# Kernel optimization log

Measured on AMD Instinct MI355X. Metric: run time of the kernel, lower is better.

Reference implementation:

```python
import jax, jax.numpy as jnp
import numpy as np

N = 50000
E = 800000
T = 16
F_NODE = 8
VOCAB = 30000
D_TXT = 64
H = 64
C = 2


def _gru_last(emb, w_ih, w_hh, b_ih, b_hh):
    # emb: [N, T, D_TXT] -> last hidden state [N, H] (PyTorch GRU equations)
    def step(h, xt):
        gi = xt @ w_ih.T + b_ih          # [N, 3H]
        gh = h @ w_hh.T + b_hh           # [N, 3H]
        i_r, i_z, i_n = jnp.split(gi, 3, axis=-1)
        h_r, h_z, h_n = jnp.split(gh, 3, axis=-1)
        r = jax.nn.sigmoid(i_r + h_r)
        z = jax.nn.sigmoid(i_z + h_z)
        n = jnp.tanh(i_n + r * h_n)
        h_new = (1.0 - z) * n + z * h
        return h_new, None
    h0 = jnp.zeros((emb.shape[0], H), dtype=emb.dtype)
    hT, _ = jax.lax.scan(step, h0, jnp.swapaxes(emb, 0, 1))
    return hT


def _gcn_norm(edge_index, n_nodes):
    # add self-loops, symmetric normalization (PyG GCNConv default)
    loops = jnp.arange(n_nodes, dtype=edge_index.dtype)
    row = jnp.concatenate([edge_index[0], loops])
    col = jnp.concatenate([edge_index[1], loops])
    deg = jax.ops.segment_sum(jnp.ones_like(col, dtype=jnp.float32), col,
                              num_segments=n_nodes)
    dinv = jax.lax.rsqrt(jnp.maximum(deg, 1.0))
    norm = dinv[row] * dinv[col]
    return row, col, norm


def _gcn_conv(x, row, col, norm, W, b, n_nodes):
    m = x @ W                                    # [N, H]
    msg = norm[:, None] * m[row]                 # gather + scale
    out = jax.ops.segment_sum(msg, col, num_segments=n_nodes)
    return out + b


def setup_inputs() -> dict:
    key = jax.random.key(0)
    ks = jax.random.split(key, 16)
    s = 0.05
    return {
        "x": jax.random.normal(ks[0], (N, F_NODE), dtype=jnp.float32),
        "edge_index": jax.random.randint(ks[1], (2, E), 0, N, dtype=jnp.int32),
        "xtext": jax.random.randint(ks[2], (N, T), 0, VOCAB, dtype=jnp.int32),
        "embed": jax.random.normal(ks[3], (VOCAB, D_TXT), dtype=jnp.float32),
        "w_ih": jax.random.normal(ks[4], (3 * H, D_TXT), dtype=jnp.float32) * s,
        "w_hh": jax.random.normal(ks[5], (3 * H, H), dtype=jnp.float32) * s,
        "b_ih": jnp.zeros((3 * H,), dtype=jnp.float32),
        "b_hh": jnp.zeros((3 * H,), dtype=jnp.float32),
        "W1": jax.random.normal(ks[6], (F_NODE + H, H), dtype=jnp.float32) * s,
        "b1": jnp.zeros((H,), dtype=jnp.float32),
        "W2": jax.random.normal(ks[7], (H, H), dtype=jnp.float32) * s,
        "b2": jnp.zeros((H,), dtype=jnp.float32),
        "Wl1": jax.random.normal(ks[8], (2 * H, H), dtype=jnp.float32) * s,
        "bl1": jnp.zeros((H,), dtype=jnp.float32),
        "Wf": jax.random.normal(ks[9], (H, C), dtype=jnp.float32) * s,
        "bf": jnp.zeros((C,), dtype=jnp.float32),
    }


def reference(x, edge_index, xtext, embed, w_ih, w_hh, b_ih, b_hh,
              W1, b1, W2, b2, Wl1, bl1, Wf, bf):
    n_nodes = x.shape[0]
    # text encode: embedding lookup + GRU, take last timestep
    emb = embed[xtext]                               # [N, T, D_TXT]
    textout = _gru_last(emb, w_ih, w_hh, b_ih, b_hh)  # [N, H]
    h = jnp.concatenate([x, textout], axis=1)        # [N, F_NODE+H]
    # two GCN layers with shared normalized edge structure
    row, col, norm = _gcn_norm(edge_index, n_nodes)
    h = jax.nn.relu(_gcn_conv(h, row, col, norm, W1, b1, n_nodes))
    h = jax.nn.relu(_gcn_conv(h, row, col, norm, W2, b2, n_nodes))
    # edge-pair classifier (original edges, no self-loops)
    xpair = jnp.concatenate([h[edge_index[0]], h[edge_index[1]]], axis=1)
    xpair = jax.nn.relu(xpair @ Wl1 + bl1)
    logits = xpair @ Wf + bf
    return jax.nn.log_softmax(logits, axis=1)
```

## Files before the change

kernel.cpp:

```cpp
#include <hip/hip_runtime.h>
#include <math.h>

#define N_NODES 50000
#define N_EDGES 800000
#define SCAN_NB ((N_NODES + 255) / 256)
#define VOCAB   30000
#define NT32    ((N_NODES + 31) / 32)

typedef __attribute__((ext_vector_type(8)))  short bf16x8;
typedef __attribute__((ext_vector_type(4)))  float f32x4;
typedef __attribute__((ext_vector_type(16))) float f32x16;
typedef __attribute__((ext_vector_type(4)))  int   i32x4;

__device__ inline short f2bf(float f) {
    union { float f; unsigned u; } v; v.f = f;
    unsigned r = v.u + 0x7FFFu + ((v.u >> 16) & 1u);
    return (short)(r >> 16);
}
__device__ inline float bflo(unsigned u) { union { unsigned u; float f; } v; v.u = u << 16; return v.f; }
__device__ inline float bfhi(unsigned u) { union { unsigned u; float f; } v; v.u = u & 0xffff0000u; return v.f; }
__device__ inline unsigned cvtpk(float a, float b) {
    unsigned r; asm("v_cvt_pk_bf16_f32 %0, %1, %2" : "=v"(r) : "v"(a), "v"(b)); return r;
}
__device__ inline float exp2neg(float x) { float r; asm("v_exp_f32 %0, -%1" : "=v"(r) : "v"(x)); return r; }
__device__ inline float exp2p(float x)   { float r; asm("v_exp_f32 %0, %1"  : "=v"(r) : "v"(x)); return r; }

__device__ inline f32x4 mfma16(bf16x8 a, bf16x8 b, f32x4 c) {
    return __builtin_amdgcn_mfma_f32_16x16x32_bf16(a, b, c, 0, 0, 0);
}
__device__ inline f32x16 mfma32(bf16x8 a, bf16x8 b, f32x16 c) {
    return __builtin_amdgcn_mfma_f32_32x32x16_bf16(a, b, c, 0, 0, 0);
}
__device__ inline f32x16 splat16(float v) {
    f32x16 r;
    #pragma unroll
    for (int i = 0; i < 16; ++i) r[i] = v;
    return r;
}
__device__ inline bf16x8 asbf(i32x4 v) { union { i32x4 i; bf16x8 b; } u; u.i = v; return u.b; }

__global__ void k_embcvt(const float* __restrict__ e, short* __restrict__ o) {
    int i = blockIdx.x * 256 + threadIdx.x;
    if (i >= VOCAB * 64 / 8) return;
    const float4* p = (const float4*)(e + i * 8);
    float4 a = p[0], b = p[1];
    bf16x8 v;
    v[0]=f2bf(a.x); v[1]=f2bf(a.y); v[2]=f2bf(a.z); v[3]=f2bf(a.w);
    v[4]=f2bf(b.x); v[5]=f2bf(b.y); v[6]=f2bf(b.z); v[7]=f2bf(b.w);
    *(bf16x8*)(o + i * 8) = v;
}

__global__ void k_count(const int* __restrict__ ei, int* __restrict__ cnt) {
    int e = blockIdx.x * 256 + threadIdx.x;
    if (e < N_EDGES) atomicAdd(&cnt[ei[N_EDGES + e]], 1);
}
__global__ void k_scan_local(const int* __restrict__ cnt, int* __restrict__ excl,
                             int* __restrict__ bsum) {
    __shared__ int s[256];
    int tid = threadIdx.x;
    int i = blockIdx.x * 256 + tid;
    int v = (i < N_NODES) ? cnt[i] : 0;
    s[tid] = v;
    __syncthreads();
    #pragma unroll
    for (int off = 1; off < 256; off <<= 1) {
        int t = (tid >= off) ? s[tid - off] : 0;
        __syncthreads();
        s[tid] += t;
        __syncthreads();
    }
    if (i < N_NODES) excl[i] = s[tid] - v;
    if (tid == 255) bsum[blockIdx.x] = s[255];
}
__global__ void k_scan_bsum(int* __restrict__ bsum) {
    __shared__ int s[256];
    int tid = threadIdx.x;
    int v = (tid < SCAN_NB) ? bsum[tid] : 0;
    s[tid] = v;
    __syncthreads();
    #pragma unroll
    for (int off = 1; off < 256; off <<= 1) {
        int t = (tid >= off) ? s[tid - off] : 0;
        __syncthreads();
        s[tid] += t;
        __syncthreads();
    }
    if (tid < SCAN_NB) bsum[tid] = s[tid] - v;
}
__global__ void k_make_starts(const int* __restrict__ excl, const int* __restrict__ bsum,
                              const int* __restrict__ cnt,
                              int* __restrict__ starts, int* __restrict__ cursor,
                              float* __restrict__ dinv) {
    int i = blockIdx.x * 256 + threadIdx.x;
    if (i >= N_NODES) return;
    int st = excl[i] + bsum[blockIdx.x];
    starts[i] = st;
    cursor[i] = st;
    dinv[i] = rsqrtf((float)cnt[i] + 1.0f);
}
__global__ void k_fill(const int* __restrict__ ei, int* __restrict__ cursor,
                       int* __restrict__ csr_src) {
    int e = blockIdx.x * 256 + threadIdx.x;
    if (e >= N_EDGES) return;
    int c = ei[N_EDGES + e];
    int p = atomicAdd(&cursor[c], 1);
    csr_src[p] = ei[e];
}

__global__ __launch_bounds__(256) void k_gru8(
    const int*   __restrict__ xtext,
    const short* __restrict__ embbf,
    const float* __restrict__ w_ih, const float* __restrict__ w_hh,
    const float* __restrict__ b_ih, const float* __restrict__ b_hh,
    unsigned* __restrict__ ht32)
{
    __shared__ short bfrag[2 * 4 * 6 * 64 * 8];
    __shared__ short hbuf[4][32 * 64];

    const int tid = threadIdx.x;
    const float L2E = 1.4426950408889634f;
    for (int u = tid; u < 3072; u += 256) {
        int l   = u & 63;
        int ct  = (u >> 6) % 6;
        int ks  = (u / 384) % 4;
        int mat = u / 1536;
        const float* W = mat ? w_hh : w_ih;
        float sc = (ct < 4) ? L2E : 2.0f * L2E;
        const float* src = &W[(ct * 32 + (l & 31)) * 64 + ks * 16 + ((l >> 5) << 3)];
        short* dst = &bfrag[u * 8];
        #pragma unroll
        for (int i = 0; i < 8; ++i) dst[i] = f2bf(src[i] * sc);
    }
    __syncthreads();

    const int lane = tid & 63;
    const int wave = tid >> 6;
    const int l5 = lane >> 5;
    const int cl = lane & 31;

    const int tile  = blockIdx.x * 4 + wave;
    if (tile >= NT32) return;
    const int nbase = tile * 32;

    float b_r[2], b_z[2], b_ni[2], b_nh[2];
    #pragma unroll
    for (int p = 0; p < 2; ++p) {
        int j = p * 32 + cl;
        b_r[p]  = (b_ih[j]        + b_hh[j])        * L2E;
        b_z[p]  = (b_ih[64 + j]   + b_hh[64 + j])   * L2E;
        b_ni[p] = b_ih[128 + j] * (2.0f * L2E);
        b_nh[p] = b_hh[128 + j] * (2.0f * L2E);
    }

    const bf16x8* BF = (const bf16x8*)bfrag;
    short* hl = &hbuf[wave][0];

    float hr0[16], hr1[16];
    #pragma unroll
    for (int g = 0; g < 16; ++g) { hr0[g] = 0.0f; hr1[g] = 0.0f; }

    const int node = min(nbase + cl, N_NODES - 1);
    const int* toks = &xtext[node * 16];

    bf16x8 eA[4], eB[4];

#define LOADE(DST, T) { int tok_ = toks[T]; const short* er_ = &embbf[tok_ * 64 + 8 * l5]; \
    DST[0] = *(const bf16x8*)(er_);      DST[1] = *(const bf16x8*)(er_ + 16); \
    DST[2] = *(const bf16x8*)(er_ + 32); DST[3] = *(const bf16x8*)(er_ + 48); }

#define STEP(T, EC, EP, FIRST, LAST) { \
    bf16x8 hA[4]; \
    if (!(FIRST)) { \
        _Pragma("unroll") \
        for (int ks = 0; ks < 4; ++ks) { \
            int o = (ks * 2 + l5) ^ (cl & 7); \
            hA[ks] = *(const bf16x8*)&hl[cl * 64 + o * 8]; \
        } \
    } \
    if (!(LAST)) LOADE(EP, (T) + 1); \
    _Pragma("unroll") \
    for (int p = 0; p < 2; ++p) { \
        f32x16 ar = splat16(b_r[p]); \
        f32x16 az = splat16(b_z[p]); \
        f32x16 ai = splat16(b_ni[p]); \
        f32x16 ah = splat16(b_nh[p]); \
        _Pragma("unroll") \
        for (int ks = 0; ks < 4; ++ks) { \
            ar = mfma32(EC[ks], BF[(ks * 6 + p) * 64 + lane], ar); \
            az = mfma32(EC[ks], BF[(ks * 6 + 2 + p) * 64 + lane], az); \
            ai = mfma32(EC[ks], BF[(ks * 6 + 4 + p) * 64 + lane], ai); \
        } \
        if (!(FIRST)) { \
            _Pragma("unroll") \
            for (int ks = 0; ks < 4; ++ks) { \
                ar = mfma32(hA[ks], BF[((4 + ks) * 6 + p) * 64 + lane], ar); \
                az = mfma32(hA[ks], BF[((4 + ks) * 6 + 2 + p) * 64 + lane], az); \
                ah = mfma32(hA[ks], BF[((4 + ks) * 6 + 4 + p) * 64 + lane], ah); \
            } \
        } \
        float* hrp = p ? hr1 : hr0; \
        _Pragma("unroll") \
        for (int g = 0; g < 16; ++g) { \
            float r = __builtin_amdgcn_rcpf(1.0f + exp2neg(ar[g])); \
            float z = __builtin_amdgcn_rcpf(1.0f + exp2neg(az[g])); \
            float v = ai[g] + r * ah[g]; \
            float n = 1.0f - 2.0f * __builtin_amdgcn_rcpf(exp2p(v) + 1.0f); \
            hrp[g] = n + z * (hrp[g] - n); \
        } \
    } \
    _Pragma("unroll") \
    for (int g = 0; g < 16; ++g) { \
        unsigned u = cvtpk(hr0[g], hr1[g]); \
        int m = (g & 3) + 8 * (g >> 2) + 4 * l5; \
        if (!(LAST)) { \
            int o0 = (cl >> 3) ^ (m & 7); \
            int o1 = (4 + (cl >> 3)) ^ (m & 7); \
            hl[m * 64 + o0 * 8 + (cl & 7)] = (short)u; \
            hl[m * 64 + o1 * 8 + (cl & 7)] = (short)(u >> 16); \
        } else { \
            int n_ = nbase + m; \
            if (n_ < N_NODES) ht32[(unsigned)n_ * 32 + cl] = u; \
        } \
    } \
}

    LOADE(eA, 0);
    STEP(0, eA, eB, true, false)

    #pragma unroll 1
    for (int tt = 0; tt < 7; ++tt) {
        int t1 = 1 + 2 * tt;
        STEP(t1,     eB, eA, false, false)
        STEP(t1 + 1, eA, eB, false, false)
    }
    STEP(15, eB, eA, false, true)

#undef STEP
#undef LOADE
}

__global__ __launch_bounds__(256) void k_mm1_mf(
    const float* __restrict__ x, const unsigned* __restrict__ ht32,
    const float* __restrict__ W1, const float* __restrict__ dinv,
    unsigned* __restrict__ msb)
{
    __shared__ short bfw[2 * 5 * 64 * 8];
    const int tid = threadIdx.x;
    for (int u = tid; u < 640; u += 256) {
        int l = u & 63, f = u >> 6;
        int ks = f % 5, p = f / 5;
        int c = p * 32 + (l & 31);
        int wl5 = l >> 5;
        short* dst = &bfw[u * 8];
        if (ks < 4) {
            const float* src = &W1[(8 + ks * 16 + 8 * wl5) * 64 + c];
            #pragma unroll
            for (int i = 0; i < 8; ++i) dst[i] = f2bf(src[i * 64]);
        } else {
            #pragma unroll
            for (int i = 0; i < 8; ++i) dst[i] = (wl5 == 0) ? f2bf(W1[i * 64 + c]) : (short)0;
        }
    }
    __syncthreads();

    const int lane = tid & 63;
    const int wave = tid >> 6;
    const int l5 = lane >> 5;
    const int cl = lane & 31;
    const int tile = blockIdx.x * 4 + wave;
    if (tile >= NT32) return;
    const int nbase = tile * 32;
    const int node = min(nbase + cl, N_NODES - 1);

    const uint4* hp = (const uint4*)(ht32 + (unsigned)node * 32);
    uint4 A0 = hp[2 * l5], A1 = hp[2 * l5 + 1];
    uint4 A2 = hp[4 + 2 * l5], A3 = hp[5 + 2 * l5];
    const float4* xp = (const float4*)(x + (size_t)node * 8);
    float4 x0 = xp[0], x1 = xp[1];

    unsigned w0[8] = {A0.x, A0.y, A0.z, A0.w, A1.x, A1.y, A1.z, A1.w};
    unsigned w1[8] = {A2.x, A2.y, A2.z, A2.w, A3.x, A3.y, A3.z, A3.w};

    bf16x8 fa[5];
    {
        i32x4 t;
        #pragma unroll
        for (int i = 0; i < 4; ++i) t[i] = (int)((w0[2*i] & 0xffffu) | (w0[2*i+1] << 16));
        fa[0] = asbf(t);
        #pragma unroll
        for (int i = 0; i < 4; ++i) t[i] = (int)((w1[2*i] & 0xffffu) | (w1[2*i+1] << 16));
        fa[1] = asbf(t);
        #pragma unroll
        for (int i = 0; i < 4; ++i) t[i] = (int)((w0[2*i] >> 16) | (w0[2*i+1] & 0xffff0000u));
        fa[2] = asbf(t);
        #pragma unroll
        for (int i = 0; i < 4; ++i) t[i] = (int)((w1[2*i] >> 16) | (w1[2*i+1] & 0xffff0000u));
        fa[3] = asbf(t);
        if (l5 == 0) {
            t[0] = (int)cvtpk(x0.x, x0.y); t[1] = (int)cvtpk(x0.z, x0.w);
            t[2] = (int)cvtpk(x1.x, x1.y); t[3] = (int)cvtpk(x1.z, x1.w);
        } else {
            t[0] = t[1] = t[2] = t[3] = 0;
        }
        fa[4] = asbf(t);
    }

    const bf16x8* BW = (const bf16x8*)bfw;
    f32x16 a0 = (f32x16)(0.0f), a1 = (f32x16)(0.0f);
    #pragma unroll
    for (int ks = 0; ks < 5; ++ks) {
        a0 = mfma32(fa[ks], BW[ks * 64 + lane], a0);
        a1 = mfma32(fa[ks], BW[(5 + ks) * 64 + lane], a1);
    }

    #pragma unroll
    for (int g = 0; g < 16; ++g) {
        int m = (g & 3) + 8 * (g >> 2) + 4 * l5;
        int n = nbase + m;
        if (n < N_NODES) {
            float dv = dinv[n];
            msb[(unsigned)n * 32 + cl] = cvtpk(a0[g] * dv, a1[g] * dv);
        }
    }
}

__global__ __launch_bounds__(256) void k_mm2_mf(
    const unsigned* __restrict__ h1b, const float* __restrict__ W2,
    const float* __restrict__ dinv, unsigned* __restrict__ msb)
{
    __shared__ short bfw[2 * 4 * 64 * 8];
    const int tid = threadIdx.x;
    for (int u = tid; u < 512; u += 256) {
        int l = u & 63, f = u >> 6;
        int ks = f & 3, p = f >> 2;
        int c = p * 32 + (l & 31);
        int wl5 = l >> 5;
        const float* src = &W2[(ks * 16 + 8 * wl5) * 64 + c];
        short* dst = &bfw[u * 8];
        #pragma unroll
        for (int i = 0; i < 8; ++i) dst[i] = f2bf(src[i * 64]);
    }
    __syncthreads();

    const int lane = tid & 63;
    const int wave = tid >> 6;
    const int l5 = lane >> 5;
    const int cl = lane & 31;
    const int tile = blockIdx.x * 4 + wave;
    if (tile >= NT32) return;
    const int nbase = tile * 32;
    const int node = min(nbase + cl, N_NODES - 1);

    const uint4* hp = (const uint4*)(h1b + (unsigned)node * 32);
    uint4 A0 = hp[2 * l5], A1 = hp[2 * l5 + 1];
    uint4 A2 = hp[4 + 2 * l5], A3 = hp[5 + 2 * l5];

    unsigned w0[8] = {A0.x, A0.y, A0.z, A0.w, A1.x, A1.y, A1.z, A1.w};
    unsigned w1[8] = {A2.x, A2.y, A2.z, A2.w, A3.x, A3.y, A3.z, A3.w};

    bf16x8 fa[4];
    {
        i32x4 t;
        #pragma unroll
        for (int i = 0; i < 4; ++i) t[i] = (int)((w0[2*i] & 0xffffu) | (w0[2*i+1] << 16));
        fa[0] = asbf(t);
        #pragma unroll
        for (int i = 0; i < 4; ++i) t[i] = (int)((w1[2*i] & 0xffffu) | (w1[2*i+1] << 16));
        fa[1] = asbf(t);
        #pragma unroll
        for (int i = 0; i < 4; ++i) t[i] = (int)((w0[2*i] >> 16) | (w0[2*i+1] & 0xffff0000u));
        fa[2] = asbf(t);
        #pragma unroll
        for (int i = 0; i < 4; ++i) t[i] = (int)((w1[2*i] >> 16) | (w1[2*i+1] & 0xffff0000u));
        fa[3] = asbf(t);
    }

    const bf16x8* BW = (const bf16x8*)bfw;
    f32x16 a0 = (f32x16)(0.0f), a1 = (f32x16)(0.0f);
    #pragma unroll
    for (int ks = 0; ks < 4; ++ks) {
        a0 = mfma32(fa[ks], BW[ks * 64 + lane], a0);
        a1 = mfma32(fa[ks], BW[(4 + ks) * 64 + lane], a1);
    }

    #pragma unroll
    for (int g = 0; g < 16; ++g) {
        int m = (g & 3) + 8 * (g >> 2) + 4 * l5;
        int n = nbase + m;
        if (n < N_NODES) {
            float dv = dinv[n];
            msb[(unsigned)n * 32 + cl] = cvtpk(a0[g] * dv, a1[g] * dv);
        }
    }
}

__global__ __launch_bounds__(256) void k_gather_p(
    const unsigned* __restrict__ msb, const int* __restrict__ csr_src,
    const int* __restrict__ starts, const int* __restrict__ cnt,
    const float* __restrict__ dinv, const float* __restrict__ b,
    unsigned* __restrict__ outp)
{
    int n = blockIdx.x * 8 + (threadIdx.x >> 5);
    if (n >= N_NODES) return;
    int w = threadIdx.x & 31;
    int c = cnt[n];
    const int* lst = csr_src + starts[n];
    unsigned us = msb[(unsigned)n * 32 + w];
    float a0 = bflo(us), a1 = bfhi(us);
    int k = 0;
    for (; k + 4 <= c; k += 4) {
        int r0 = lst[k], r1 = lst[k+1], r2 = lst[k+2], r3 = lst[k+3];
        unsigned u0 = msb[(unsigned)r0 * 32 + w];
        unsigned u1 = msb[(unsigned)r1 * 32 + w];
        unsigned u2 = msb[(unsigned)r2 * 32 + w];
        unsigned u3 = msb[(unsigned)r3 * 32 + w];
        a0 += bflo(u0) + bflo(u1) + bflo(u2) + bflo(u3);
        a1 += bfhi(u0) + bfhi(u1) + bfhi(u2) + bfhi(u3);
    }
    for (; k < c; ++k) {
        unsigned u = msb[(unsigned)lst[k] * 32 + w];
        a0 += bflo(u); a1 += bfhi(u);
    }
    float d = dinv[n];
    float v0 = fmaxf(d * a0 + b[w], 0.0f);
    float v1 = fmaxf(d * a1 + b[w + 32], 0.0f);
    outp[(unsigned)n * 32 + w] = cvtpk(v0, v1);
}

__global__ __launch_bounds__(256) void k_gather_h2(
    const unsigned* __restrict__ msb, const int* __restrict__ csr_src,
    const int* __restrict__ starts, const int* __restrict__ cnt,
    const float* __restrict__ dinv, const float* __restrict__ b,
    short* __restrict__ out)
{
    int n = blockIdx.x * 8 + (threadIdx.x >> 5);
    if (n >= N_NODES) return;
    int w = threadIdx.x & 31;
    int c = cnt[n];
    const int* lst = csr_src + starts[n];
    unsigned us = msb[(unsigned)n * 32 + w];
    float a0 = bflo(us), a1 = bfhi(us);
    int k = 0;
    for (; k + 4 <= c; k += 4) {
        int r0 = lst[k], r1 = lst[k+1], r2 = lst[k+2], r3 = lst[k+3];
        unsigned u0 = msb[(unsigned)r0 * 32 + w];
        unsigned u1 = msb[(unsigned)r1 * 32 + w];
        unsigned u2 = msb[(unsigned)r2 * 32 + w];
        unsigned u3 = msb[(unsigned)r3 * 32 + w];
        a0 += bflo(u0) + bflo(u1) + bflo(u2) + bflo(u3);
        a1 += bfhi(u0) + bfhi(u1) + bfhi(u2) + bfhi(u3);
    }
    for (; k < c; ++k) {
        unsigned u = msb[(unsigned)lst[k] * 32 + w];
        a0 += bflo(u); a1 += bfhi(u);
    }
    float d = dinv[n];
    float v0 = fmaxf(d * a0 + b[w], 0.0f);
    float v1 = fmaxf(d * a1 + b[w + 32], 0.0f);
    unsigned u = cvtpk(v0, v1);
    out[(unsigned)n * 64 + w]      = (short)u;
    out[(unsigned)n * 64 + 32 + w] = (short)(u >> 16);
}

__global__ __launch_bounds__(256) void k_edge_mfma(
    const int* __restrict__ ei, const short* __restrict__ h2b,
    const float* __restrict__ Wl1, const float* __restrict__ bl1,
    const float* __restrict__ Wf,  const float* __restrict__ bf,
    float* __restrict__ out)
{
    __shared__ float wl_s[128 * 64];
    const int tid = threadIdx.x;
    for (int i = tid; i < 128 * 64; i += 256) wl_s[i] = Wl1[i];
    __syncthreads();

    const int lane = tid & 63;
    const int wave = tid >> 6;
    const int lg = lane >> 4;
    const int ll = lane & 15;

    bf16x8 B[16];
    #pragma unroll
    for (int ks = 0; ks < 4; ++ks) {
        #pragma unroll
        for (int ct = 0; ct < 4; ++ct) {
            int c  = ct * 16 + ll;
            int kb = ks * 32 + 8 * lg;
            bf16x8 v;
            #pragma unroll
            for (int i = 0; i < 8; ++i) v[i] = f2bf(wl_s[(kb + i) * 64 + c]);
            B[ks * 4 + ct] = v;
        }
    }
    float wf0[4], wf1[4], bl[4];
    #pragma unroll
    for (int ct = 0; ct < 4; ++ct) {
        int c = ct * 16 + ll;
        wf0[ct] = Wf[c * 2 + 0];
        wf1[ct] = Wf[c * 2 + 1];
        bl[ct]  = bl1[c];
    }
    const float bf0 = bf[0], bf1 = bf[1];

    for (int tile = blockIdx.x * 4 + wave; tile < N_EDGES / 16; tile += gridDim.x * 4) {
        const int ebase = tile * 16;
        const int erow  = ebase + ll;
        const int src = ei[erow];
        const int dst = ei[N_EDGES + erow];

        f32x4 acc[4];
        #pragma unroll
        for (int ct = 0; ct < 4; ++ct) acc[ct] = (f32x4){bl[ct], bl[ct], bl[ct], bl[ct]};

        #pragma unroll
        for (int ks = 0; ks < 4; ++ks) {
            const int nd = (ks < 2) ? src : dst;
            bf16x8 A = *(const bf16x8*)&h2b[nd * 64 + (ks & 1) * 32 + 8 * lg];
            #pragma unroll
            for (int ct = 0; ct < 4; ++ct) acc[ct] = mfma16(A, B[ks * 4 + ct], acc[ct]);
        }

        float p0[4], p1[4];
        #pragma unroll
        for (int q = 0; q < 4; ++q) { p0[q] = 0.0f; p1[q] = 0.0f; }
        #pragma unroll
        for (int ct = 0; ct < 4; ++ct) {
            #pragma unroll
            for (int q = 0; q < 4; ++q) {
                float hd = fmaxf(acc[ct][q], 0.0f);
                p0[q] += hd * wf0[ct];
                p1[q] += hd * wf1[ct];
            }
        }
        #pragma unroll
        for (int m = 1; m <= 8; m <<= 1) {
            #pragma unroll
            for (int q = 0; q < 4; ++q) {
                p0[q] += __shfl_xor(p0[q], m, 64);
                p1[q] += __shfl_xor(p1[q], m, 64);
            }
        }
        if (ll < 8) {
            int q = ll >> 1, cls = ll & 1;
            float l0 = p0[q] + bf0, l1 = p1[q] + bf1;
            float mx  = fmaxf(l0, l1);
            float lse = mx + __logf(__expf(l0 - mx) + __expf(l1 - mx));
            float val = (cls ? l1 : l0) - lse;
            out[(ebase + 4 * lg + q) * 2 + cls] = val;
        }
    }
}

extern "C" void kernel_launch(void* const* d_in, const int* in_sizes, int n_in,
                              void* d_out, int out_size, void* d_ws, size_t ws_size,
                              hipStream_t stream) {
    const float* x     = (const float*)d_in[0];
    const int*   ei    = (const int*)  d_in[1];
    const int*   xtext = (const int*)  d_in[2];
    const float* embed = (const float*)d_in[3];
    const float* w_ih  = (const float*)d_in[4];
    const float* w_hh  = (const float*)d_in[5];
    const float* b_ih  = (const float*)d_in[6];
    const float* b_hh  = (const float*)d_in[7];
    const float* W1    = (const float*)d_in[8];
    const float* b1    = (const float*)d_in[9];
    const float* W2    = (const float*)d_in[10];
    const float* b2    = (const float*)d_in[11];
    const float* Wl1   = (const float*)d_in[12];
    const float* bl1   = (const float*)d_in[13];
    const float* Wf    = (const float*)d_in[14];
    const float* bf    = (const float*)d_in[15];
    float* out = (float*)d_out;

    char* ws = (char*)d_ws;
    size_t off = 0;
    auto alloc = [&](size_t bytes) { char* p = ws + off; off += (bytes + 255) & ~size_t(255); return p; };
    unsigned* ht32   = (unsigned*)alloc(N_NODES * 32 * 4);
    unsigned* msb    = (unsigned*)alloc(N_NODES * 32 * 4);
    unsigned* h1b    = (unsigned*)alloc(N_NODES * 32 * 4);
    short*    h2b    = (short*)   alloc(N_NODES * 64 * 2);
    float*    dinv   = (float*)   alloc(N_NODES * 4);
    int*      cnt    = (int*)     alloc(N_NODES * 4);
    int*      excl   = (int*)     alloc(N_NODES * 4);
    int*      starts = (int*)     alloc(N_NODES * 4);
    int*      cursor = (int*)     alloc(N_NODES * 4);
    int*      bsum   = (int*)     alloc(SCAN_NB * 4);
    int*      csr_src= (int*)     alloc(N_EDGES * 4);
    short*    embbf  = (short*)   alloc(VOCAB * 64 * 2);

    k_embcvt<<<(VOCAB * 64 / 8 + 255) / 256, 256, 0, stream>>>(embed, embbf);

    hipMemsetAsync(cnt, 0, N_NODES * 4, stream);
    k_count<<<(N_EDGES + 255) / 256, 256, 0, stream>>>(ei, cnt);
    k_scan_local<<<SCAN_NB, 256, 0, stream>>>(cnt, excl, bsum);
    k_scan_bsum<<<1, 256, 0, stream>>>(bsum);
    k_make_starts<<<SCAN_NB, 256, 0, stream>>>(excl, bsum, cnt, starts, cursor, dinv);
    k_fill<<<(N_EDGES + 255) / 256, 256, 0, stream>>>(ei, cursor, csr_src);

    k_gru8<<<(NT32 + 3) / 4, 256, 0, stream>>>(xtext, embbf, w_ih, w_hh, b_ih, b_hh, ht32);

    k_mm1_mf<<<(NT32 + 3) / 4, 256, 0, stream>>>(x, ht32, W1, dinv, msb);
    k_gather_p<<<(N_NODES + 7) / 8, 256, 0, stream>>>(msb, csr_src, starts, cnt, dinv, b1, h1b);

    k_mm2_mf<<<(NT32 + 3) / 4, 256, 0, stream>>>(h1b, W2, dinv, msb);
    k_gather_h2<<<(N_NODES + 7) / 8, 256, 0, stream>>>(msb, csr_src, starts, cnt, dinv, b2, h2b);

    k_edge_mfma<<<2048, 256, 0, stream>>>(ei, h2b, Wl1, bl1, Wf, bf, out);
}
```

Baseline: 307.2 us.

## Precompute per-token input-gate table and split GRU hidden units across two waves

```diff
diff --git a/kernel.cpp b/kernel.cpp
--- a/kernel.cpp
+++ b/kernel.cpp
@@ -6,6 +6,7 @@
 #define SCAN_NB ((N_NODES + 255) / 256)
 #define VOCAB   30000
 #define NT32    ((N_NODES + 31) / 32)
+#define NTT     ((VOCAB + 31) / 32)
 
 typedef __attribute__((ext_vector_type(8)))  short bf16x8;
 typedef __attribute__((ext_vector_type(4)))  float f32x4;
@@ -31,24 +32,7 @@
 __device__ inline f32x16 mfma32(bf16x8 a, bf16x8 b, f32x16 c) {
     return __builtin_amdgcn_mfma_f32_32x32x16_bf16(a, b, c, 0, 0, 0);
 }
-__device__ inline f32x16 splat16(float v) {
-    f32x16 r;
-    #pragma unroll
-    for (int i = 0; i < 16; ++i) r[i] = v;
-    return r;
-}
 __device__ inline bf16x8 asbf(i32x4 v) { union { i32x4 i; bf16x8 b; } u; u.i = v; return u.b; }
-
-__global__ void k_embcvt(const float* __restrict__ e, short* __restrict__ o) {
-    int i = blockIdx.x * 256 + threadIdx.x;
-    if (i >= VOCAB * 64 / 8) return;
-    const float4* p = (const float4*)(e + i * 8);
-    float4 a = p[0], b = p[1];
-    bf16x8 v;
-    v[0]=f2bf(a.x); v[1]=f2bf(a.y); v[2]=f2bf(a.z); v[3]=f2bf(a.w);
-    v[4]=f2bf(b.x); v[5]=f2bf(b.y); v[6]=f2bf(b.z); v[7]=f2bf(b.w);
-    *(bf16x8*)(o + i * 8) = v;
-}
 
 __global__ void k_count(const int* __restrict__ ei, int* __restrict__ cnt) {
     int e = blockIdx.x * 256 + threadIdx.x;
@@ -107,27 +91,22 @@
     csr_src[p] = ei[e];
 }
 
-__global__ __launch_bounds__(256) void k_gru8(
-    const int*   __restrict__ xtext,
-    const short* __restrict__ embbf,
-    const float* __restrict__ w_ih, const float* __restrict__ w_hh,
+__global__ __launch_bounds__(256) void k_gitab(
+    const float* __restrict__ embed,
+    const float* __restrict__ w_ih,
     const float* __restrict__ b_ih, const float* __restrict__ b_hh,
-    unsigned* __restrict__ ht32)
+    float* __restrict__ tab)
 {
-    __shared__ short bfrag[2 * 4 * 6 * 64 * 8];
-    __shared__ short hbuf[4][32 * 64];
-
+    __shared__ short bfw[24 * 64 * 8];
     const int tid = threadIdx.x;
     const float L2E = 1.4426950408889634f;
-    for (int u = tid; u < 3072; u += 256) {
-        int l   = u & 63;
-        int ct  = (u >> 6) % 6;
-        int ks  = (u / 384) % 4;
-        int mat = u / 1536;
-        const float* W = mat ? w_hh : w_ih;
-        float sc = (ct < 4) ? L2E : 2.0f * L2E;
-        const float* src = &W[(ct * 32 + (l & 31)) * 64 + ks * 16 + ((l >> 5) << 3)];
-        short* dst = &bfrag[u * 8];
+    for (int u = tid; u < 1536; u += 256) {
+        int l = u & 63, f = u >> 6;
+        int ks = f & 3, pp = (f >> 2) & 1, gate = f >> 3;
+        float sc = (gate < 2) ? L2E : 2.0f * L2E;
+        int c = gate * 64 + pp * 32 + (l & 31);
+        const float* src = &w_ih[c * 64 + 16 * ks + ((l >> 5) << 3)];
+        short* dst = &bfw[u * 8];
         #pragma unroll
         for (int i = 0; i < 8; ++i) dst[i] = f2bf(src[i] * sc);
     }
@@ -137,106 +116,173 @@
     const int wave = tid >> 6;
     const int l5 = lane >> 5;
     const int cl = lane & 31;
-
-    const int tile  = blockIdx.x * 4 + wave;
-    if (tile >= NT32) return;
-    const int nbase = tile * 32;
-
-    float b_r[2], b_z[2], b_ni[2], b_nh[2];
-    #pragma unroll
-    for (int p = 0; p < 2; ++p) {
-        int j = p * 32 + cl;
-        b_r[p]  = (b_ih[j]        + b_hh[j])        * L2E;
-        b_z[p]  = (b_ih[64 + j]   + b_hh[64 + j])   * L2E;
-        b_ni[p] = b_ih[128 + j] * (2.0f * L2E);
-        b_nh[p] = b_hh[128 + j] * (2.0f * L2E);
-    }
-
-    const bf16x8* BF = (const bf16x8*)bfrag;
-    short* hl = &hbuf[wave][0];
-
-    float hr0[16], hr1[16];
-    #pragma unroll
-    for (int g = 0; g < 16; ++g) { hr0[g] = 0.0f; hr1[g] = 0.0f; }
-
-    const int node = min(nbase + cl, N_NODES - 1);
-    const int* toks = &xtext[node * 16];
-
-    bf16x8 eA[4], eB[4];
-
-#define LOADE(DST, T) { int tok_ = toks[T]; const short* er_ = &embbf[tok_ * 64 + 8 * l5]; \
-    DST[0] = *(const bf16x8*)(er_);      DST[1] = *(const bf16x8*)(er_ + 16); \
-    DST[2] = *(const bf16x8*)(er_ + 32); DST[3] = *(const bf16x8*)(er_ + 48); }
-
-#define STEP(T, EC, EP, FIRST, LAST) { \
-    bf16x8 hA[4]; \
-    if (!(FIRST)) { \
-        _Pragma("unroll") \
-        for (int ks = 0; ks < 4; ++ks) { \
-            int o = (ks * 2 + l5) ^ (cl & 7); \
-            hA[ks] = *(const bf16x8*)&hl[cl * 64 + o * 8]; \
-        } \
-    } \
-    if (!(LAST)) LOADE(EP, (T) + 1); \
-    _Pragma("unroll") \
-    for (int p = 0; p < 2; ++p) { \
-        f32x16 ar = splat16(b_r[p]); \
-        f32x16 az = splat16(b_z[p]); \
-        f32x16 ai = splat16(b_ni[p]); \
-        f32x16 ah = splat16(b_nh[p]); \
-        _Pragma("unroll") \
-        for (int ks = 0; ks < 4; ++ks) { \
-            ar = mfma32(EC[ks], BF[(ks * 6 + p) * 64 + lane], ar); \
-            az = mfma32(EC[ks], BF[(ks * 6 + 2 + p) * 64 + lane], az); \
-            ai = mfma32(EC[ks], BF[(ks * 6 + 4 + p) * 64 + lane], ai); \
-        } \
-        if (!(FIRST)) { \
-            _Pragma("unroll") \
-            for (int ks = 0; ks < 4; ++ks) { \
-                ar = mfma32(hA[ks], BF[((4 + ks) * 6 + p) * 64 + lane], ar); \
-                az = mfma32(hA[ks], BF[((4 + ks) * 6 + 2 + p) * 64 + lane], az); \
-                ah = mfma32(hA[ks], BF[((4 + ks) * 6 + 4 + p) * 64 + lane], ah); \
-            } \
-        } \
-        float* hrp = p ? hr1 : hr0; \
-        _Pragma("unroll") \
-        for (int g = 0; g < 16; ++g) { \
-            float r = __builtin_amdgcn_rcpf(1.0f + exp2neg(ar[g])); \
-            float z = __builtin_amdgcn_rcpf(1.0f + exp2neg(az[g])); \
-            float v = ai[g] + r * ah[g]; \
-            float n = 1.0f - 2.0f * __builtin_amdgcn_rcpf(exp2p(v) + 1.0f); \
-            hrp[g] = n + z * (hrp[g] - n); \
-        } \
-    } \
-    _Pragma("unroll") \
-    for (int g = 0; g < 16; ++g) { \
-        unsigned u = cvtpk(hr0[g], hr1[g]); \
-        int m = (g & 3) + 8 * (g >> 2) + 4 * l5; \
-        if (!(LAST)) { \
-            int o0 = (cl >> 3) ^ (m & 7); \
-            int o1 = (4 + (cl >> 3)) ^ (m & 7); \
-            hl[m * 64 + o0 * 8 + (cl & 7)] = (short)u; \
-            hl[m * 64 + o1 * 8 + (cl & 7)] = (short)(u >> 16); \
-        } else { \
-            int n_ = nbase + m; \
-            if (n_ < N_NODES) ht32[(unsigned)n_ * 32 + cl] = u; \
-        } \
-    } \
-}
-
-    LOADE(eA, 0);
-    STEP(0, eA, eB, true, false)
+    const int tile = blockIdx.x * 4 + wave;
+    if (tile >= NTT) return;
+    const int tok = min(tile * 32 + cl, VOCAB - 1);
+
+    bf16x8 fa[4];
+    #pragma unroll
+    for (int ks = 0; ks < 4; ++ks) {
+        const float4* p = (const float4*)&embed[tok * 64 + 16 * ks + 8 * l5];
+        float4 a = p[0], b = p[1];
+        i32x4 t;
+        t[0] = (int)cvtpk(a.x, a.y); t[1] = (int)cvtpk(a.z, a.w);
+        t[2] = (int)cvtpk(b.x, b.y); t[3] = (int)cvtpk(b.z, b.w);
+        fa[ks] = asbf(t);
+    }
+
+    const bf16x8* BW = (const bf16x8*)bfw;
+    f32x16 a00 = (f32x16)(0.0f), a01 = (f32x16)(0.0f);
+    f32x16 a10 = (f32x16)(0.0f), a11 = (f32x16)(0.0f);
+    f32x16 a20 = (f32x16)(0.0f), a21 = (f32x16)(0.0f);
+    #pragma unroll
+    for (int ks = 0; ks < 4; ++ks) {
+        a00 = mfma32(fa[ks], BW[(0 * 4 + ks) * 64 + lane], a00);
+        a01 = mfma32(fa[ks], BW[(1 * 4 + ks) * 64 + lane], a01);
+        a10 = mfma32(fa[ks], BW[(2 * 4 + ks) * 64 + lane], a10);
+        a11 = mfma32(fa[ks], BW[(3 * 4 + ks) * 64 + lane], a11);
+        a20 = mfma32(fa[ks], BW[(4 * 4 + ks) * 64 + lane], a20);
+        a21 = mfma32(fa[ks], BW[(5 * 4 + ks) * 64 + lane], a21);
+    }
+
+    float bv[6];
+    #pragma unroll
+    for (int gate = 0; gate < 3; ++gate)
+        #pragma unroll
+        for (int pp = 0; pp < 2; ++pp) {
+            int d = gate * 64 + pp * 32 + cl;
+            bv[gate * 2 + pp] = (gate < 2) ? (b_ih[d] + b_hh[d]) * L2E
+                                           : b_ih[d] * (2.0f * L2E);
+        }
+
+    #pragma unroll
+    for (int g = 0; g < 16; ++g) {
+        int m = (g & 3) + 8 * (g >> 2) + 4 * l5;
+        int tokr = tile * 32 + m;
+        if (tokr < VOCAB) {
+            float* row = tab + (unsigned)tokr * 192;
+            row[cl]            = a00[g] + bv[0];
+            row[32 + cl]       = a01[g] + bv[1];
+            row[64 + cl]       = a10[g] + bv[2];
+            row[96 + cl]       = a11[g] + bv[3];
+            row[128 + cl]      = a20[g] + bv[4];
+            row[160 + cl]      = a21[g] + bv[5];
+        }
+    }
+}
+
+__global__ __launch_bounds__(256) void k_gru12(
+    const int*   __restrict__ xtext,
+    const float* __restrict__ tab,
+    const float* __restrict__ w_hh, const float* __restrict__ b_hh,
+    unsigned* __restrict__ ht32)
+{
+    __shared__ short whh[24 * 64 * 8];
+    __shared__ short hbuf[2][32 * 64];
+    __shared__ int   tokl[2][512];
+
+    const int tid = threadIdx.x;
+    const float L2E = 1.4426950408889634f;
+    for (int u = tid; u < 1536; u += 256) {
+        int l = u & 63, f = u >> 6;
+        int ks = f & 3, pp = (f >> 2) & 1, gate = f >> 3;
+        float sc = (gate < 2) ? L2E : 2.0f * L2E;
+        int c = gate * 64 + pp * 32 + (l & 31);
+        const float* src = &w_hh[c * 64 + 16 * ks + ((l >> 5) << 3)];
+        short* dst = &whh[u * 8];
+        #pragma unroll
+        for (int i = 0; i < 8; ++i) dst[i] = f2bf(src[i] * sc);
+    }
+    for (int u = tid; u < 1024; u += 256) {
+        int tb_ = u >> 9, idx = u & 511;
+        int tG_ = min(blockIdx.x * 2 + tb_, NT32 - 1);
+        int node = min(tG_ * 32 + (idx >> 4), N_NODES - 1);
+        tokl[tb_][idx] = xtext[node * 16 + (idx & 15)];
+    }
+    __syncthreads();
+
+    const int lane = tid & 63;
+    const int wave = tid >> 6;
+    const int l5 = lane >> 5;
+    const int cl = lane & 31;
+    const int tb = wave >> 1;
+    const int pp = wave & 1;
+    const int tG = min(blockIdx.x * 2 + tb, NT32 - 1);
+    const int nbase = tG * 32;
+
+    const float bnh = b_hh[128 + pp * 32 + cl] * (2.0f * L2E);
+    const bf16x8* WH = (const bf16x8*)whh;
+    short* hl = &hbuf[tb][0];
+    const int* tkp = &tokl[tb][0];
+    const int dofs = pp * 32 + cl;
+
+    float hr[16];
+    #pragma unroll
+    for (int g = 0; g < 16; ++g) hr[g] = 0.0f;
 
     #pragma unroll 1
-    for (int tt = 0; tt < 7; ++tt) {
-        int t1 = 1 + 2 * tt;
-        STEP(t1,     eB, eA, false, false)
-        STEP(t1 + 1, eA, eB, false, false)
-    }
-    STEP(15, eB, eA, false, true)
-
-#undef STEP
-#undef LOADE
+    for (int t = 0; t < 16; ++t) {
+        float tr[16], tz[16], tn[16];
+        #pragma unroll
+        for (int g = 0; g < 16; ++g) {
+            int m = (g & 3) + 8 * (g >> 2) + 4 * l5;
+            int tk = tkp[m * 16 + t];
+            const float* row = tab + (unsigned)tk * 192 + dofs;
+            tr[g] = row[0];
+            tz[g] = row[64];
+            tn[g] = row[128];
+        }
+        __syncthreads();
+        bf16x8 hA[4];
+        if (t > 0) {
+            #pragma unroll
+            for (int ks = 0; ks < 4; ++ks) {
+                int o = (ks * 2 + l5) ^ (cl & 7);
+                hA[ks] = *(const bf16x8*)&hl[cl * 64 + o * 8];
+            }
+        }
+        __syncthreads();
+
+        f32x16 ar, az, ah;
+        #pragma unroll
+        for (int g = 0; g < 16; ++g) { ar[g] = tr[g]; az[g] = tz[g]; ah[g] = bnh; }
+        if (t > 0) {
+            #pragma unroll
+            for (int ks = 0; ks < 4; ++ks) {
+                ar = mfma32(hA[ks], WH[((0 * 2 + pp) * 4 + ks) * 64 + lane], ar);
+                az = mfma32(hA[ks], WH[((1 * 2 + pp) * 4 + ks) * 64 + lane], az);
+                ah = mfma32(hA[ks], WH[((2 * 2 + pp) * 4 + ks) * 64 + lane], ah);
+            }
+        }
+        #pragma unroll
+        for (int g = 0; g < 16; ++g) {
+            float r = __builtin_amdgcn_rcpf(1.0f + exp2neg(ar[g]));
+            float z = __builtin_amdgcn_rcpf(1.0f + exp2neg(az[g]));
+            float v = tn[g] + r * ah[g];
+            float n = 1.0f - 2.0f * __builtin_amdgcn_rcpf(exp2p(v) + 1.0f);
+            float h = n + z * (hr[g] - n);
+            hr[g] = h;
+            int m = (g & 3) + 8 * (g >> 2) + 4 * l5;
+            int j = dofs;
+            int o = (j >> 3) ^ (m & 7);
+            hl[m * 64 + o * 8 + (j & 7)] = (short)cvtpk(h, h);
+        }
+    }
+    __syncthreads();
+
+    if (pp == 0 && (blockIdx.x * 2 + tb) < NT32) {
+        #pragma unroll
+        for (int g = 0; g < 16; ++g) {
+            int m = (g & 3) + 8 * (g >> 2) + 4 * l5;
+            int n_ = nbase + m;
+            if (n_ < N_NODES) {
+                int o1 = (4 + (cl >> 3)) ^ (m & 7);
+                unsigned hi = (unsigned)(unsigned short)hl[m * 64 + o1 * 8 + (cl & 7)];
+                unsigned lo = (unsigned)(unsigned short)(short)cvtpk(hr[g], hr[g]);
+                ht32[(unsigned)n_ * 32 + cl] = lo | (hi << 16);
+            }
+        }
+    }
 }
 
 __global__ __launch_bounds__(256) void k_mm1_mf(
@@ -585,9 +631,9 @@
     int*      cursor = (int*)     alloc(N_NODES * 4);
     int*      bsum   = (int*)     alloc(SCAN_NB * 4);
     int*      csr_src= (int*)     alloc(N_EDGES * 4);
-    short*    embbf  = (short*)   alloc(VOCAB * 64 * 2);
-
-    k_embcvt<<<(VOCAB * 64 / 8 + 255) / 256, 256, 0, stream>>>(embed, embbf);
+    float*    tab    = (float*)   alloc((size_t)VOCAB * 192 * 4);
+
+    k_gitab<<<(NTT + 3) / 4, 256, 0, stream>>>(embed, w_ih, b_ih, b_hh, tab);
 
     hipMemsetAsync(cnt, 0, N_NODES * 4, stream);
     k_count<<<(N_EDGES + 255) / 256, 256, 0, stream>>>(ei, cnt);
@@ -596,7 +642,7 @@
     k_make_starts<<<SCAN_NB, 256, 0, stream>>>(excl, bsum, cnt, starts, cursor, dinv);
     k_fill<<<(N_EDGES + 255) / 256, 256, 0, stream>>>(ei, cursor, csr_src);
 
-    k_gru8<<<(NT32 + 3) / 4, 256, 0, stream>>>(xtext, embbf, w_ih, w_hh, b_ih, b_hh, ht32);
+    k_gru12<<<(NT32 + 1) / 2, 256, 0, stream>>>(xtext, tab, w_hh, b_hh, ht32);
 
     k_mm1_mf<<<(NT32 + 3) / 4, 256, 0, stream>>>(x, ht32, W1, dinv, msb);
     k_gather_p<<<(N_NODES + 7) / 8, 256, 0, stream>>>(msb, csr_src, starts, cnt, dinv, b1, h1b);
```

After: 311.2 us. No clear change (+1.3%).
